# Performance work log

Hardware: AMD Instinct MI355X
Metric: run time of the kernel (lower is better)

## Reference

```python
import jax, jax.numpy as jnp
import numpy as np

N_NODES = 4096
N_EDGES = 8192
N_GRAPHS = 256
D_NODE = 64
D_EDGE = 32
H = 256


def setup_inputs() -> dict:
    key = jax.random.key(0)
    ks = jax.random.split(key, 16)
    s = lambda d: 1.0 / np.sqrt(d)
    inp = {
        "x": jax.random.normal(ks[0], (N_NODES, D_NODE), dtype=jnp.float32),
        "edge_index": jax.random.randint(ks[1], (2, N_EDGES), 0, N_NODES),
        "edge_attr": jax.random.normal(ks[2], (N_EDGES, D_EDGE), dtype=jnp.float32),
        "batch": jnp.sort(jax.random.randint(ks[3], (N_NODES,), 0, N_GRAPHS)),
        # conv1: edge MLP 32 -> 64*256, root weight 64->256, bias 256
        "nn1_w": jax.random.normal(ks[4], (D_EDGE, D_NODE * H), dtype=jnp.float32) * s(D_EDGE),
        "nn1_b": jnp.zeros((D_NODE * H,), dtype=jnp.float32),
        "root1_w": jax.random.normal(ks[5], (D_NODE, H), dtype=jnp.float32) * s(D_NODE),
        "bias1": jnp.zeros((H,), dtype=jnp.float32),
        # conv2: edge MLP 32 -> 256*256, root weight 256->256, bias 256
        "nn2_w": jax.random.normal(ks[6], (D_EDGE, H * H), dtype=jnp.float32) * s(D_EDGE),
        "nn2_b": jnp.zeros((H * H,), dtype=jnp.float32),
        "root2_w": jax.random.normal(ks[7], (H, H), dtype=jnp.float32) * s(H),
        "bias2": jnp.zeros((H,), dtype=jnp.float32),
        # readout MLP: 256 -> 128 -> 1
        "lin1_w": jax.random.normal(ks[8], (H, H // 2), dtype=jnp.float32) * s(H),
        "lin1_b": jnp.zeros((H // 2,), dtype=jnp.float32),
        "lin2_w": jax.random.normal(ks[9], (H // 2, 1), dtype=jnp.float32) * s(H // 2),
        "lin2_b": jnp.zeros((1,), dtype=jnp.float32),
    }
    return inp


def nnconv(x, src, dst, edge_attr, nn_w, nn_b, root_w, bias, out_c):
    # PyG NNConv (aggr='add'): per-edge weight matrix from edge MLP,
    # message = x[src] @ W_e, scatter-add at dst, plus root transform + bias.
    e = edge_attr.shape[0]
    in_c = x.shape[1]
    w_e = (edge_attr @ nn_w + nn_b).reshape(e, in_c, out_c)  # [E, in, out]
    msg = jnp.einsum('ei,eio->eo', x[src], w_e)              # [E, out]
    agg = jax.ops.segment_sum(msg, dst, num_segments=x.shape[0])
    return agg + x @ root_w + bias


def reference(x, edge_index, edge_attr, batch,
              nn1_w, nn1_b, root1_w, bias1,
              nn2_w, nn2_b, root2_w, bias2,
              lin1_w, lin1_b, lin2_w, lin2_b):
    src, dst = edge_index[0], edge_index[1]
    h = nnconv(x, src, dst, edge_attr, nn1_w, nn1_b, root1_w, bias1, H)
    h = jax.nn.relu(h)
    h = nnconv(h, src, dst, edge_attr, nn2_w, nn2_b, root2_w, bias2, H)
    # global mean pool over graphs
    sums = jax.ops.segment_sum(h, batch, num_segments=N_GRAPHS)
    cnts = jax.ops.segment_sum(jnp.ones((h.shape[0],), h.dtype), batch, num_segments=N_GRAPHS)
    pooled = sums / jnp.maximum(cnts, 1.0)[:, None]
    # dropout is identity in eval mode
    z = jax.nn.relu(pooled @ lin1_w + lin1_b)
    return jax.nn.sigmoid(z @ lin2_w + lin2_b)  # [N_GRAPHS, 1]
```

## Files before the change

kernel.cpp:

```cpp
#include <hip/hip_runtime.h>
#include <math.h>

#define N_NODES 4096
#define N_EDGES 8192
#define N_GRAPHS 256
#define D_NODE 64
#define D_EDGE 32
#define HH 256

#define K1 2176
#define K2 8704
#define NC1 34
#define NC2 136
#define NSL1 8
#define NSL2 16

typedef _Float16 half8v __attribute__((ext_vector_type(8)));
typedef _Float16 half4v __attribute__((ext_vector_type(4)));
typedef float floatx4 __attribute__((ext_vector_type(4)));

static const size_t OFF_S    = 0;
static const size_t OFF_BT1  = 17825792;
static const size_t OFF_BT2  = 18104320;
static const size_t OFF_CP   = 19218432;
static const size_t OFF_H    = 25509888;
static const size_t OFF_INT  = 26034176;
static const size_t OFF_POOL = 26050560;

__device__ void csr_body(const int* __restrict__ dst,
                         int* __restrict__ starts,
                         int* __restrict__ elist) {
    __shared__ int cnt[4096];
    __shared__ int ps[256];
    int t = threadIdx.x;
#pragma unroll
    for (int i = 0; i < 16; ++i) cnt[t * 16 + i] = 0;
    __syncthreads();
#pragma unroll
    for (int i = 0; i < 32; ++i) atomicAdd(&cnt[dst[i * 256 + t]], 1);
    __syncthreads();
    int v[16]; int s = 0;
#pragma unroll
    for (int i = 0; i < 16; ++i) { v[i] = cnt[t * 16 + i]; s += v[i]; }
    ps[t] = s;
    __syncthreads();
    for (int off = 1; off < 256; off <<= 1) {
        int tv = (t >= off) ? ps[t - off] : 0;
        __syncthreads();
        ps[t] += tv;
        __syncthreads();
    }
    int excl = ps[t] - s;
#pragma unroll
    for (int i = 0; i < 16; ++i) {
        starts[t * 16 + i] = excl;
        cnt[t * 16 + i] = excl;
        excl += v[i];
    }
    if (t == 255) starts[4096] = excl;
    __syncthreads();
#pragma unroll
    for (int i = 0; i < 32; ++i) {
        int e = i * 256 + t;
        int d = dst[e];
        int p = atomicAdd(&cnt[d], 1);
        elist[p] = e;
    }
}

__device__ void packT_body(const float* __restrict__ w,
                           const float* __restrict__ b,
                           const float* __restrict__ rw,
                           _Float16* __restrict__ BT,
                           int kk0, int o0, int K,
                           int wlim, int blim, int wshift, int wmask, int wrow) {
    __shared__ float T[64][65];
    int t = threadIdx.x;
    int ol = t & 63, kb = t >> 6;
#pragma unroll
    for (int p = 0; p < 16; ++p) {
        int kl = p * 4 + kb;
        int kk = kk0 + kl, o = o0 + ol;
        float v;
        if (kk < wlim)      v = w[(kk >> wshift) * wrow + (kk & wmask) * 256 + o];
        else if (kk < blim) v = b[(kk - wlim) * 256 + o];
        else                v = rw[(kk - blim) * 256 + o];
        T[kl][ol] = v;
    }
    __syncthreads();
    int kl2 = t & 63, ob = t >> 6;
#pragma unroll
    for (int p = 0; p < 16; ++p) {
        int ol2 = p * 4 + ob;
        BT[(size_t)(o0 + ol2) * K + kk0 + kl2] = (_Float16)T[kl2][ol2];
    }
}

__global__ __launch_bounds__(256) void prep_k(const int* __restrict__ dst,
                                              int* __restrict__ starts,
                                              int* __restrict__ elist,
                                              const float* __restrict__ w1,
                                              const float* __restrict__ b1,
                                              const float* __restrict__ r1,
                                              const float* __restrict__ w2,
                                              const float* __restrict__ b2,
                                              const float* __restrict__ r2,
                                              _Float16* __restrict__ BT1,
                                              _Float16* __restrict__ BT2) {
    int bx = blockIdx.x, by = blockIdx.y;
    if (bx == 0) {
        if (by == 0) csr_body(dst, starts, elist);
        return;
    }
    int pbx = bx - 1, o0 = by * 64;
    if (pbx < NC1)
        packT_body(w1, b1, r1, BT1, pbx * 64, o0, K1, 2048, 2112, 6, 63, 16384);
    else
        packT_body(w2, b2, r2, BT2, (pbx - NC1) * 64, o0, K2, 8192, 8448, 8, 255, 65536);
}

__global__ __launch_bounds__(64) void s1_k(const float* __restrict__ x,
                                           const float* __restrict__ ea,
                                           const int* __restrict__ src,
                                           const int* __restrict__ starts,
                                           const int* __restrict__ elist,
                                           _Float16* __restrict__ S) {
    int n = blockIdx.x, t = threadIdx.x;
    int cg = t & 7, kg = t >> 3;
    int i0 = cg * 8;
    float acc[5][8] = {};
    int e0 = starts[n], e1 = starts[n + 1];
    for (int ie = e0; ie < e1; ++ie) {
        int e = elist[ie];
        int sn = src[e];
        float4 f0 = *(const float4*)&x[sn * 64 + i0];
        float4 f1 = *(const float4*)&x[sn * 64 + i0 + 4];
        float xv[8] = {f0.x, f0.y, f0.z, f0.w, f1.x, f1.y, f1.z, f1.w};
#pragma unroll
        for (int j = 0; j < 4; ++j) {
            float va = ea[e * 32 + kg + 8 * j];
#pragma unroll
            for (int c = 0; c < 8; ++c) acc[j][c] += va * xv[c];
        }
        if (kg == 0) {
#pragma unroll
            for (int c = 0; c < 8; ++c) acc[4][c] += xv[c];
        }
    }
    _Float16* row = S + (size_t)n * K1;
#pragma unroll
    for (int j = 0; j < 4; ++j) {
        int k = kg + 8 * j;
        half8v o;
#pragma unroll
        for (int c = 0; c < 8; ++c) o[c] = (_Float16)acc[j][c];
        *(half8v*)&row[k * 64 + i0] = o;
    }
    if (kg == 0) {
        half8v o;
#pragma unroll
        for (int c = 0; c < 8; ++c) o[c] = (_Float16)acc[4][c];
        *(half8v*)&row[32 * 64 + i0] = o;
    }
    if (kg == 1) {
        float4 f0 = *(const float4*)&x[n * 64 + i0];
        float4 f1 = *(const float4*)&x[n * 64 + i0 + 4];
        half8v o;
        o[0] = (_Float16)f0.x; o[1] = (_Float16)f0.y; o[2] = (_Float16)f0.z; o[3] = (_Float16)f0.w;
        o[4] = (_Float16)f1.x; o[5] = (_Float16)f1.y; o[6] = (_Float16)f1.z; o[7] = (_Float16)f1.w;
        *(half8v*)&row[2112 + i0] = o;
    }
}

__global__ __launch_bounds__(256) void s2_k(const _Float16* __restrict__ h,
                                            const float* __restrict__ ea,
                                            const int* __restrict__ src,
                                            const int* __restrict__ starts,
                                            const int* __restrict__ elist,
                                            _Float16* __restrict__ S) {
    int n = blockIdx.x, t = threadIdx.x;
    int cg = t & 31, kg = t >> 5;
    int i0 = cg * 8;
    float acc[5][8] = {};
    int e0 = starts[n], e1 = starts[n + 1];
    for (int ie = e0; ie < e1; ++ie) {
        int e = elist[ie];
        int sn = src[e];
        half8v hv = *(const half8v*)&h[sn * 256 + i0];
        float xv[8];
#pragma unroll
        for (int c = 0; c < 8; ++c) xv[c] = (float)hv[c];
#pragma unroll
        for (int j = 0; j < 4; ++j) {
            float va = ea[e * 32 + kg + 8 * j];
#pragma unroll
            for (int c = 0; c < 8; ++c) acc[j][c] += va * xv[c];
        }
        if (kg == 0) {
#pragma unroll
            for (int c = 0; c < 8; ++c) acc[4][c] += xv[c];
        }
    }
    _Float16* row = S + (size_t)n * K2;
#pragma unroll
    for (int j = 0; j < 4; ++j) {
        int k = kg + 8 * j;
        half8v o;
#pragma unroll
        for (int c = 0; c < 8; ++c) o[c] = (_Float16)acc[j][c];
        *(half8v*)&row[k * 256 + i0] = o;
    }
    if (kg == 0) {
        half8v o;
#pragma unroll
        for (int c = 0; c < 8; ++c) o[c] = (_Float16)acc[4][c];
        *(half8v*)&row[32 * 256 + i0] = o;
    }
    if (kg == 1) {
        half8v hv = *(const half8v*)&h[n * 256 + i0];
        *(half8v*)&row[8448 + i0] = hv;
    }
}

__device__ __forceinline__ void async_copy16(const void* g, void* l) {
    __builtin_amdgcn_global_load_lds(
        (__attribute__((address_space(1))) unsigned int*)(g),
        (__attribute__((address_space(3))) unsigned int*)(l), 16, 0, 0);
}

__global__ __launch_bounds__(256, 3) void gemm_f16(const _Float16* __restrict__ A,
                                                   const _Float16* __restrict__ BT,
                                                   _Float16* __restrict__ Cpart,
                                                   int K, int NC, int Z) {
    __shared__ _Float16 lds[17408];
    _Float16* As = lds;
    _Float16* Bs = lds + 128 * 64;
    int tid = threadIdx.x;
    int w = tid >> 6, l = tid & 63;
    int mt = blockIdx.y, nt = blockIdx.x, z = blockIdx.z;
    int c0 = z * NC / Z, c1 = (z + 1) * NC / Z;
    int k0 = c0 * 64;
    int wm = w & 1, wn = w >> 1;

    int lr = l >> 3, lc = l & 7;
    int gc = lc ^ lr;
    const _Float16* gA0 = A  + (size_t)(mt * 128 + w * 32 + lr) * K + k0 + gc * 8;
    const _Float16* gB0 = BT + (size_t)(nt * 128 + w * 32 + lr) * K + k0 + gc * 8;

    int lm = l & 15, q4 = l >> 4;
    int sw = lm & 7;

    floatx4 acc[4][4] = {};

    for (int s = c0; s < c1; ++s) {
#pragma unroll
        for (int q = 0; q < 4; ++q) {
            async_copy16(gA0 + (size_t)q * 8 * K, As + (w * 32 + q * 8) * 64);
            async_copy16(gB0 + (size_t)q * 8 * K, Bs + (w * 32 + q * 8) * 64);
        }
        gA0 += 64; gB0 += 64;
        __syncthreads();
#pragma unroll
        for (int kw = 0; kw < 2; ++kw) {
            int ck = ((kw * 4 + q4) ^ sw) * 8;
            half8v af[4], bf[4];
#pragma unroll
            for (int i = 0; i < 4; ++i)
                af[i] = *(const half8v*)&As[(wm * 64 + i * 16 + lm) * 64 + ck];
#pragma unroll
            for (int j = 0; j < 4; ++j)
                bf[j] = *(const half8v*)&Bs[(wn * 64 + j * 16 + lm) * 64 + ck];
#pragma unroll
            for (int i = 0; i < 4; ++i)
#pragma unroll
                for (int j = 0; j < 4; ++j)
                    acc[i][j] = __builtin_amdgcn_mfma_f32_16x16x32_f16(af[i], bf[j], acc[i][j], 0, 0, 0);
        }
        __syncthreads();
    }

    _Float16* ep = lds + w * 4352;
#pragma unroll
    for (int i = 0; i < 4; ++i)
#pragma unroll
        for (int j = 0; j < 4; ++j)
#pragma unroll
            for (int r = 0; r < 4; ++r)
                ep[(i * 16 + q4 * 4 + r) * 68 + j * 16 + lm] = (_Float16)acc[i][j][r];
    __syncthreads();
    _Float16* Cp = Cpart + (size_t)z * (N_NODES * HH);
    int row8 = l >> 3, colg = (l & 7) * 8;
    int gm0 = mt * 128 + wm * 64, gn0 = nt * 128 + wn * 64;
#pragma unroll
    for (int i8 = 0; i8 < 8; ++i8) {
        int rr = i8 * 8 + row8;
        half4v lo = *(const half4v*)&ep[rr * 68 + colg];
        half4v hi = *(const half4v*)&ep[rr * 68 + colg + 4];
        half8v v;
        v[0] = lo[0]; v[1] = lo[1]; v[2] = lo[2]; v[3] = lo[3];
        v[4] = hi[0]; v[5] = hi[1]; v[6] = hi[2]; v[7] = hi[3];
        *(half8v*)&Cp[(size_t)(gm0 + rr) * HH + gn0 + colg] = v;
    }
}

__global__ __launch_bounds__(512, 4) void gemm2_k(const _Float16* __restrict__ A,
                                                  const _Float16* __restrict__ BT,
                                                  const int* __restrict__ batch,
                                                  float* __restrict__ pool,
                                                  int K, int NC, int Z) {
    __shared__ _Float16 lds[34816];
    __shared__ int gids[128];
    _Float16* As = lds;
    _Float16* Bs = lds + 128 * 64;
    int tid = threadIdx.x;
    int w = tid >> 6, l = tid & 63;
    int mt = blockIdx.x, z = blockIdx.y;
    int c0 = z * NC / Z, c1 = (z + 1) * NC / Z;
    int k0 = c0 * 64;
    int wm = w & 1, wn = w >> 1;

    int lr = l >> 3, lc = l & 7;
    int gc = lc ^ lr;
    const _Float16* gA0 = A  + (size_t)(mt * 128 + w * 16 + lr) * K + k0 + gc * 8;
    const _Float16* gB0 = BT + (size_t)(w * 32 + lr) * K + k0 + gc * 8;

    int lm = l & 15, q4 = l >> 4;
    int sw = lm & 7;

    floatx4 acc[4][4] = {};

    for (int s = c0; s < c1; ++s) {
#pragma unroll
        for (int q = 0; q < 2; ++q)
            async_copy16(gA0 + (size_t)q * 8 * K, As + (w * 16 + q * 8) * 64);
#pragma unroll
        for (int q = 0; q < 4; ++q)
            async_copy16(gB0 + (size_t)q * 8 * K, Bs + (w * 32 + q * 8) * 64);
        gA0 += 64; gB0 += 64;
        __syncthreads();
#pragma unroll
        for (int kw = 0; kw < 2; ++kw) {
            int ck = ((kw * 4 + q4) ^ sw) * 8;
            half8v af[4], bf[4];
#pragma unroll
            for (int i = 0; i < 4; ++i)
                af[i] = *(const half8v*)&As[(wm * 64 + i * 16 + lm) * 64 + ck];
#pragma unroll
            for (int j = 0; j < 4; ++j)
                bf[j] = *(const half8v*)&Bs[(wn * 64 + j * 16 + lm) * 64 + ck];
#pragma unroll
            for (int i = 0; i < 4; ++i)
#pragma unroll
                for (int j = 0; j < 4; ++j)
                    acc[i][j] = __builtin_amdgcn_mfma_f32_16x16x32_f16(af[i], bf[j], acc[i][j], 0, 0, 0);
        }
        __syncthreads();
    }

    _Float16* ep = lds + w * 4352;
#pragma unroll
    for (int i = 0; i < 4; ++i)
#pragma unroll
        for (int j = 0; j < 4; ++j)
#pragma unroll
            for (int r = 0; r < 4; ++r)
                ep[(i * 16 + q4 * 4 + r) * 68 + j * 16 + lm] = (_Float16)acc[i][j][r];
    if (tid < 128) gids[tid] = batch[mt * 128 + tid];
    __syncthreads();

    int gn0 = wn * 64;
    int gbase = wm * 64;
    int gprev = gids[gbase];
    float run = 0.f;
    for (int rr = 0; rr < 64; ++rr) {
        float v = (float)ep[rr * 68 + l];
        int g = gids[gbase + rr];
        if (g != gprev) {
            atomicAdd(&pool[gprev * 256 + gn0 + l], run);
            run = 0.f; gprev = g;
        }
        run += v;
    }
    atomicAdd(&pool[gprev * 256 + gn0 + l], run);
}

__global__ __launch_bounds__(256) void hep_k(const _Float16* __restrict__ Cp,
                                             const float* __restrict__ bias,
                                             _Float16* __restrict__ h,
                                             float* __restrict__ pool) {
    if (blockIdx.x < 256) pool[blockIdx.x * 256 + threadIdx.x] = 0.f;
    int idx = (blockIdx.x * 256 + threadIdx.x) * 8;
    float a[8] = {};
#pragma unroll
    for (int zz = 0; zz < NSL1; ++zz) {
        half8v v = *(const half8v*)(Cp + (size_t)zz * (N_NODES * HH) + idx);
#pragma unroll
        for (int j = 0; j < 8; ++j) a[j] += (float)v[j];
    }
    int col = idx & 255;
    half8v o;
#pragma unroll
    for (int j = 0; j < 8; ++j) o[j] = (_Float16)fmaxf(a[j] + bias[col + j], 0.f);
    *(half8v*)(h + idx) = o;
}

__global__ __launch_bounds__(256) void readout_k(const float* __restrict__ pool,
                                                 const int* __restrict__ batch,
                                                 const float* __restrict__ bias2,
                                                 const float* __restrict__ l1w,
                                                 const float* __restrict__ l1b,
                                                 const float* __restrict__ l2w,
                                                 const float* __restrict__ l2b,
                                                 float* __restrict__ out) {
    int g = blockIdx.x, t = threadIdx.x;
    __shared__ int bnds[2];
    __shared__ float sp[256];
    __shared__ float sz[128];
    if (t < 2) {
        int target = g + t;
        int lo = 0, hi = N_NODES;
        while (lo < hi) { int mid = (lo + hi) >> 1; if (batch[mid] < target) lo = mid + 1; else hi = mid; }
        bnds[t] = lo;
    }
    __syncthreads();
    int lo = bnds[0], hi = bnds[1];
    sp[t] = (hi > lo) ? (pool[g * 256 + t] / (float)(hi - lo) + bias2[t]) : 0.f;
    __syncthreads();
    if (t < 128) {
        float a = l1b[t];
#pragma unroll 8
        for (int i = 0; i < 256; ++i) a += sp[i] * l1w[i * 128 + t];
        sz[t] = fmaxf(a, 0.f) * l2w[t];
    }
    __syncthreads();
    for (int ss = 64; ss > 0; ss >>= 1) {
        if (t < ss) sz[t] += sz[t + ss];
        __syncthreads();
    }
    if (t == 0) {
        float zz = sz[0] + l2b[0];
        out[g] = 1.0f / (1.0f + expf(-zz));
    }
}

extern "C" void kernel_launch(void* const* d_in, const int* in_sizes, int n_in,
                              void* d_out, int out_size, void* d_ws, size_t ws_size,
                              hipStream_t stream) {
    const float* x       = (const float*)d_in[0];
    const int*   ei      = (const int*)d_in[1];
    const float* ea      = (const float*)d_in[2];
    const int*   batch   = (const int*)d_in[3];
    const float* nn1_w   = (const float*)d_in[4];
    const float* nn1_b   = (const float*)d_in[5];
    const float* root1_w = (const float*)d_in[6];
    const float* bias1   = (const float*)d_in[7];
    const float* nn2_w   = (const float*)d_in[8];
    const float* nn2_b   = (const float*)d_in[9];
    const float* root2_w = (const float*)d_in[10];
    const float* bias2   = (const float*)d_in[11];
    const float* lin1_w  = (const float*)d_in[12];
    const float* lin1_b  = (const float*)d_in[13];
    const float* lin2_w  = (const float*)d_in[14];
    const float* lin2_b  = (const float*)d_in[15];
    float* out = (float*)d_out;
    float* ws  = (float*)d_ws;

    _Float16* S   = (_Float16*)(ws + OFF_S);
    _Float16* BT1 = (_Float16*)(ws + OFF_BT1);
    _Float16* BT2 = (_Float16*)(ws + OFF_BT2);
    _Float16* Cp  = (_Float16*)(ws + OFF_CP);
    _Float16* h   = (_Float16*)(ws + OFF_H);
    int* ip     = (int*)(ws + OFF_INT);
    int* starts = ip;
    int* elist  = ip + 4100;
    float* pool = ws + OFF_POOL;

    const int* srcv = ei;
    const int* dstv = ei + N_EDGES;

    prep_k<<<dim3(1 + NC1 + NC2, 4), 256, 0, stream>>>(
        dstv, starts, elist, nn1_w, nn1_b, root1_w, nn2_w, nn2_b, root2_w, BT1, BT2);

    s1_k<<<4096, 64, 0, stream>>>(x, ea, srcv, starts, elist, S);

    gemm_f16<<<dim3(2, 32, NSL1), 256, 0, stream>>>(S, BT1, Cp, K1, NC1, NSL1);

    hep_k<<<512, 256, 0, stream>>>(Cp, bias1, h, pool);

    s2_k<<<4096, 256, 0, stream>>>(h, ea, srcv, starts, elist, S);

    gemm2_k<<<dim3(32, NSL2), 512, 0, stream>>>(S, BT2, batch, pool, K2, NC2, NSL2);

    readout_k<<<N_GRAPHS, 256, 0, stream>>>(pool, batch, bias2,
                                            lin1_w, lin1_b, lin2_w, lin2_b, out);
}
```

Measured before the change: 184.1 us.

## Pool per graph before second NNConv GEMM to shrink its M dimension

Since the second NNConv layer and the mean pool are both linear, the per-node edge-feature outer products are summed per graph before the GEMM rather than after. The new sg_k builds one augmented K2-length row per graph, including the summed root-term features. A 256-row split-K GEMM then writes fp32 partials, which readout reduces. This removes most of the large second GEMM and the atomic pooling, at the cost of a per-graph aggregation kernel with only 256 blocks that loop serially over each graph's edges.

```diff
diff --git a/kernel.cpp b/kernel.cpp
--- a/kernel.cpp
+++ b/kernel.cpp
@@ -13,7 +13,8 @@
 #define NC1 34
 #define NC2 136
 #define NSL1 8
-#define NSL2 16
+#define NSL3 32
+#define CHUNK 64
 
 typedef _Float16 half8v __attribute__((ext_vector_type(8)));
 typedef _Float16 half4v __attribute__((ext_vector_type(4)));
@@ -25,7 +26,6 @@
 static const size_t OFF_CP   = 19218432;
 static const size_t OFF_H    = 25509888;
 static const size_t OFF_INT  = 26034176;
-static const size_t OFF_POOL = 26050560;
 
 __device__ void csr_body(const int* __restrict__ dst,
                          int* __restrict__ starts,
@@ -172,56 +172,6 @@
     }
 }
 
-__global__ __launch_bounds__(256) void s2_k(const _Float16* __restrict__ h,
-                                            const float* __restrict__ ea,
-                                            const int* __restrict__ src,
-                                            const int* __restrict__ starts,
-                                            const int* __restrict__ elist,
-                                            _Float16* __restrict__ S) {
-    int n = blockIdx.x, t = threadIdx.x;
-    int cg = t & 31, kg = t >> 5;
-    int i0 = cg * 8;
-    float acc[5][8] = {};
-    int e0 = starts[n], e1 = starts[n + 1];
-    for (int ie = e0; ie < e1; ++ie) {
-        int e = elist[ie];
-        int sn = src[e];
-        half8v hv = *(const half8v*)&h[sn * 256 + i0];
-        float xv[8];
-#pragma unroll
-        for (int c = 0; c < 8; ++c) xv[c] = (float)hv[c];
-#pragma unroll
-        for (int j = 0; j < 4; ++j) {
-            float va = ea[e * 32 + kg + 8 * j];
-#pragma unroll
-            for (int c = 0; c < 8; ++c) acc[j][c] += va * xv[c];
-        }
-        if (kg == 0) {
-#pragma unroll
-            for (int c = 0; c < 8; ++c) acc[4][c] += xv[c];
-        }
-    }
-    _Float16* row = S + (size_t)n * K2;
-#pragma unroll
-    for (int j = 0; j < 4; ++j) {
-        int k = kg + 8 * j;
-        half8v o;
-#pragma unroll
-        for (int c = 0; c < 8; ++c) o[c] = (_Float16)acc[j][c];
-        *(half8v*)&row[k * 256 + i0] = o;
-    }
-    if (kg == 0) {
-        half8v o;
-#pragma unroll
-        for (int c = 0; c < 8; ++c) o[c] = (_Float16)acc[4][c];
-        *(half8v*)&row[32 * 256 + i0] = o;
-    }
-    if (kg == 1) {
-        half8v hv = *(const half8v*)&h[n * 256 + i0];
-        *(half8v*)&row[8448 + i0] = hv;
-    }
-}
-
 __device__ __forceinline__ void async_copy16(const void* g, void* l) {
     __builtin_amdgcn_global_load_lds(
         (__attribute__((address_space(1))) unsigned int*)(g),
@@ -303,26 +253,94 @@
     }
 }
 
-__global__ __launch_bounds__(512, 4) void gemm2_k(const _Float16* __restrict__ A,
+__global__ __launch_bounds__(256) void hep_k(const _Float16* __restrict__ Cp,
+                                             const float* __restrict__ bias,
+                                             _Float16* __restrict__ h) {
+    int idx = (blockIdx.x * 256 + threadIdx.x) * 8;
+    float a[8] = {};
+#pragma unroll
+    for (int zz = 0; zz < NSL1; ++zz) {
+        half8v v = *(const half8v*)(Cp + (size_t)zz * (N_NODES * HH) + idx);
+#pragma unroll
+        for (int j = 0; j < 8; ++j) a[j] += (float)v[j];
+    }
+    int col = idx & 255;
+    half8v o;
+#pragma unroll
+    for (int j = 0; j < 8; ++j) o[j] = (_Float16)fmaxf(a[j] + bias[col + j], 0.f);
+    *(half8v*)(h + idx) = o;
+}
+
+__global__ __launch_bounds__(256) void sg_k(const _Float16* __restrict__ h,
+                                            const float* __restrict__ ea,
+                                            const int* __restrict__ src,
+                                            const int* __restrict__ starts,
+                                            const int* __restrict__ elist,
+                                            const int* __restrict__ batch,
+                                            _Float16* __restrict__ SG) {
+    int g = blockIdx.x, t = threadIdx.x;
+    __shared__ int bnds[2];
+    __shared__ int sl[CHUNK];
+    __shared__ float eaS[CHUNK * 32];
+    __shared__ _Float16 hS[CHUNK * 256];
+    if (t < 2) {
+        int target = g + t;
+        int lo = 0, hi = N_NODES;
+        while (lo < hi) { int mid = (lo + hi) >> 1; if (batch[mid] < target) lo = mid + 1; else hi = mid; }
+        bnds[t] = lo;
+    }
+    __syncthreads();
+    int nlo = bnds[0], nhi = bnds[1];
+    int e0 = starts[nlo], e1 = starts[nhi];
+    float acc[33];
+#pragma unroll
+    for (int k = 0; k < 33; ++k) acc[k] = 0.f;
+    for (int base = e0; base < e1; base += CHUNK) {
+        int ne = min(CHUNK, e1 - base);
+        if (t < ne) { int e = elist[base + t]; sl[t] = src[e]; }
+        __syncthreads();
+        for (int j = t; j < ne * 32; j += 256) {
+            int e = elist[base + (j >> 5)];
+            eaS[j] = ea[e * 32 + (j & 31)];
+        }
+        for (int ie = 0; ie < ne; ++ie)
+            hS[ie * 256 + t] = h[(size_t)sl[ie] * 256 + t];
+        __syncthreads();
+        for (int ie = 0; ie < ne; ++ie) {
+            float hv = (float)hS[ie * 256 + t];
+            const float* er = &eaS[ie * 32];
+#pragma unroll 8
+            for (int k = 0; k < 32; ++k) acc[k] += er[k] * hv;
+            acc[32] += hv;
+        }
+        __syncthreads();
+    }
+    float aug = 0.f;
+    for (int n = nlo; n < nhi; ++n) aug += (float)h[(size_t)n * 256 + t];
+    _Float16* row = SG + (size_t)g * K2;
+#pragma unroll
+    for (int k = 0; k < 33; ++k) row[k * 256 + t] = (_Float16)acc[k];
+    row[8448 + t] = (_Float16)aug;
+}
+
+__global__ __launch_bounds__(256, 3) void gemm_sg(const _Float16* __restrict__ A,
                                                   const _Float16* __restrict__ BT,
-                                                  const int* __restrict__ batch,
-                                                  float* __restrict__ pool,
+                                                  float* __restrict__ Cp,
                                                   int K, int NC, int Z) {
-    __shared__ _Float16 lds[34816];
-    __shared__ int gids[128];
+    __shared__ _Float16 lds[16384];
     _Float16* As = lds;
     _Float16* Bs = lds + 128 * 64;
     int tid = threadIdx.x;
     int w = tid >> 6, l = tid & 63;
-    int mt = blockIdx.x, z = blockIdx.y;
+    int mt = blockIdx.y, nt = blockIdx.x, z = blockIdx.z;
     int c0 = z * NC / Z, c1 = (z + 1) * NC / Z;
     int k0 = c0 * 64;
     int wm = w & 1, wn = w >> 1;
 
     int lr = l >> 3, lc = l & 7;
     int gc = lc ^ lr;
-    const _Float16* gA0 = A  + (size_t)(mt * 128 + w * 16 + lr) * K + k0 + gc * 8;
-    const _Float16* gB0 = BT + (size_t)(w * 32 + lr) * K + k0 + gc * 8;
+    const _Float16* gA0 = A  + (size_t)(mt * 128 + w * 32 + lr) * K + k0 + gc * 8;
+    const _Float16* gB0 = BT + (size_t)(nt * 128 + w * 32 + lr) * K + k0 + gc * 8;
 
     int lm = l & 15, q4 = l >> 4;
     int sw = lm & 7;
@@ -331,11 +349,10 @@
 
     for (int s = c0; s < c1; ++s) {
 #pragma unroll
-        for (int q = 0; q < 2; ++q)
-            async_copy16(gA0 + (size_t)q * 8 * K, As + (w * 16 + q * 8) * 64);
-#pragma unroll
-        for (int q = 0; q < 4; ++q)
+        for (int q = 0; q < 4; ++q) {
+            async_copy16(gA0 + (size_t)q * 8 * K, As + (w * 32 + q * 8) * 64);
             async_copy16(gB0 + (size_t)q * 8 * K, Bs + (w * 32 + q * 8) * 64);
+        }
         gA0 += 64; gB0 += 64;
         __syncthreads();
 #pragma unroll
@@ -357,54 +374,18 @@
         __syncthreads();
     }
 
-    _Float16* ep = lds + w * 4352;
+    float* C = Cp + (size_t)z * (N_GRAPHS * HH);
+    int gm0 = mt * 128 + wm * 64, gn0 = nt * 128 + wn * 64;
 #pragma unroll
     for (int i = 0; i < 4; ++i)
 #pragma unroll
         for (int j = 0; j < 4; ++j)
 #pragma unroll
             for (int r = 0; r < 4; ++r)
-                ep[(i * 16 + q4 * 4 + r) * 68 + j * 16 + lm] = (_Float16)acc[i][j][r];
-    if (tid < 128) gids[tid] = batch[mt * 128 + tid];
-    __syncthreads();
-
-    int gn0 = wn * 64;
-    int gbase = wm * 64;
-    int gprev = gids[gbase];
-    float run = 0.f;
-    for (int rr = 0; rr < 64; ++rr) {
-        float v = (float)ep[rr * 68 + l];
-        int g = gids[gbase + rr];
-        if (g != gprev) {
-            atomicAdd(&pool[gprev * 256 + gn0 + l], run);
-            run = 0.f; gprev = g;
-        }
-        run += v;
-    }
-    atomicAdd(&pool[gprev * 256 + gn0 + l], run);
-}
-
-__global__ __launch_bounds__(256) void hep_k(const _Float16* __restrict__ Cp,
-                                             const float* __restrict__ bias,
-                                             _Float16* __restrict__ h,
-                                             float* __restrict__ pool) {
-    if (blockIdx.x < 256) pool[blockIdx.x * 256 + threadIdx.x] = 0.f;
-    int idx = (blockIdx.x * 256 + threadIdx.x) * 8;
-    float a[8] = {};
-#pragma unroll
-    for (int zz = 0; zz < NSL1; ++zz) {
-        half8v v = *(const half8v*)(Cp + (size_t)zz * (N_NODES * HH) + idx);
-#pragma unroll
-        for (int j = 0; j < 8; ++j) a[j] += (float)v[j];
-    }
-    int col = idx & 255;
-    half8v o;
-#pragma unroll
-    for (int j = 0; j < 8; ++j) o[j] = (_Float16)fmaxf(a[j] + bias[col + j], 0.f);
-    *(half8v*)(h + idx) = o;
-}
-
-__global__ __launch_bounds__(256) void readout_k(const float* __restrict__ pool,
+                C[(size_t)(gm0 + i * 16 + q4 * 4 + r) * HH + gn0 + j * 16 + lm] = acc[i][j][r];
+}
+
+__global__ __launch_bounds__(256) void readout_k(const float* __restrict__ CpS,
                                                  const int* __restrict__ batch,
                                                  const float* __restrict__ bias2,
                                                  const float* __restrict__ l1w,
@@ -424,7 +405,11 @@
     }
     __syncthreads();
     int lo = bnds[0], hi = bnds[1];
-    sp[t] = (hi > lo) ? (pool[g * 256 + t] / (float)(hi - lo) + bias2[t]) : 0.f;
+    float s = 0.f;
+#pragma unroll
+    for (int zz = 0; zz < NSL3; ++zz)
+        s += CpS[(size_t)zz * (N_GRAPHS * HH) + g * 256 + t];
+    sp[t] = (hi > lo) ? (s / (float)(hi - lo) + bias2[t]) : 0.f;
     __syncthreads();
     if (t < 128) {
         float a = l1b[t];
@@ -469,11 +454,11 @@
     _Float16* BT1 = (_Float16*)(ws + OFF_BT1);
     _Float16* BT2 = (_Float16*)(ws + OFF_BT2);
     _Float16* Cp  = (_Float16*)(ws + OFF_CP);
+    float*    CpS = ws + OFF_CP;
     _Float16* h   = (_Float16*)(ws + OFF_H);
     int* ip     = (int*)(ws + OFF_INT);
     int* starts = ip;
     int* elist  = ip + 4100;
-    float* pool = ws + OFF_POOL;
 
     const int* srcv = ei;
     const int* dstv = ei + N_EDGES;
@@ -485,12 +470,12 @@
 
     gemm_f16<<<dim3(2, 32, NSL1), 256, 0, stream>>>(S, BT1, Cp, K1, NC1, NSL1);
 
-    hep_k<<<512, 256, 0, stream>>>(Cp, bias1, h, pool);
-
-    s2_k<<<4096, 256, 0, stream>>>(h, ea, srcv, starts, elist, S);
-
-    gemm2_k<<<dim3(32, NSL2), 512, 0, stream>>>(S, BT2, batch, pool, K2, NC2, NSL2);
-
-    readout_k<<<N_GRAPHS, 256, 0, stream>>>(pool, batch, bias2,
+    hep_k<<<512, 256, 0, stream>>>(Cp, bias1, h);
+
+    sg_k<<<N_GRAPHS, 256, 0, stream>>>(h, ea, srcv, starts, elist, batch, S);
+
+    gemm_sg<<<dim3(2, 2, NSL3), 256, 0, stream>>>(S, BT2, CpS, K2, NC2, NSL3);
+
+    readout_k<<<N_GRAPHS, 256, 0, stream>>>(CpS, batch, bias2,
                                             lin1_w, lin1_b, lin2_w, lin2_b, out);
 }
```

Measured after the change: 283.4 us. 53.9% more time.
